# Optimization experiments

Measured on AMD Instinct MI355X. Metric: run time of the kernel, lower is better.

Reference implementation:

```python
import jax, jax.numpy as jnp
import numpy as np

FP8_MAX = 448.0  # float8_e4m3fn max (use_e4m3=True)
K, N = 512, 512


def setup_inputs() -> dict:
    key = jax.random.key(0)
    kx, kw = jax.random.split(key)
    x = jax.random.normal(kx, (8, 8192, K), dtype=jnp.float32)
    weight = jax.random.normal(kw, (K, N), dtype=jnp.float32) * 0.02
    return {"x": x, "weight": weight}


def reference(x, weight):
    B, S, _ = x.shape
    x2d = x.reshape(-1, K)  # [M, K]

    # dynamic per-tensor quantization of activations to fp8 e4m3
    x_amax = jnp.max(jnp.abs(x2d))
    x_scale = FP8_MAX / jnp.maximum(x_amax, 1e-12)
    x_fp8 = jnp.clip(x2d * x_scale, -FP8_MAX, FP8_MAX).astype(jnp.float8_e4m3fn)

    # dynamic per-tensor quantization of weight (transposed, as in source)
    w_amax = jnp.max(jnp.abs(weight))
    w_scale = FP8_MAX / jnp.maximum(w_amax, 1e-12)
    w_fp8 = jnp.clip(weight.T * w_scale, -FP8_MAX, FP8_MAX).astype(jnp.float8_e4m3fn)  # [N, K]

    # cast-up matmul then dequantize with combined inverse scale
    res = jnp.matmul(x_fp8.astype(jnp.float32), w_fp8.astype(jnp.float32).T)  # [M, N]
    out = res * ((1.0 / x_scale) * (1.0 / w_scale))
    return out.reshape(B, S, N).astype(x.dtype)
```

## Files before the change

### kernel.cpp

```cpp
#include <hip/hip_runtime.h>

typedef float f32x4 __attribute__((ext_vector_type(4)));
typedef long i64;

#define KDIM 512
#define NDIM 512
#define LDS_STRIDE 520
#define OUT_STRIDE 260

__device__ __forceinline__ float clamp448(float v) {
    return fminf(fmaxf(v, -448.0f), 448.0f);
}

__global__ __launch_bounds__(256) void amax_kernel(const float4* __restrict__ x,
                                                   const float4* __restrict__ w,
                                                   unsigned* __restrict__ scales) {
    const int tid = threadIdx.x;
    float m = 0.0f;
    if (blockIdx.x < 4096) {
        int base = blockIdx.x * 256 + tid;
        #pragma unroll
        for (int j = 0; j < 8; ++j) {
            float4 v = x[base + j * 1048576];
            m = fmaxf(m, fmaxf(fmaxf(fabsf(v.x), fabsf(v.y)), fmaxf(fabsf(v.z), fabsf(v.w))));
        }
    } else {
        int base = (blockIdx.x - 4096) * 256 + tid;
        #pragma unroll
        for (int j = 0; j < 8; ++j) {
            float4 v = w[base + j * 8192];
            m = fmaxf(m, fmaxf(fmaxf(fabsf(v.x), fabsf(v.y)), fmaxf(fabsf(v.z), fabsf(v.w))));
        }
    }
    #pragma unroll
    for (int off = 32; off > 0; off >>= 1)
        m = fmaxf(m, __shfl_down(m, off, 64));
    __shared__ float red[4];
    const int wave = tid >> 6, lane = tid & 63;
    if (lane == 0) red[wave] = m;
    __syncthreads();
    if (tid == 0) {
        m = fmaxf(fmaxf(red[0], red[1]), fmaxf(red[2], red[3]));
        atomicMax(&scales[blockIdx.x < 4096 ? 0 : 1], __float_as_uint(m));
    }
}

__global__ __launch_bounds__(256) void wquant_kernel(const float4* __restrict__ wv,
                                                     const unsigned* __restrict__ scales,
                                                     unsigned char* __restrict__ wq) {
    const float ws = 448.0f / fmaxf(__uint_as_float(scales[1]), 1e-12f);
    #pragma unroll
    for (int j = 0; j < 4; ++j) {
        const int idx = blockIdx.x * 1024 + j * 256 + threadIdx.x;
        const int k = idx >> 7;
        const int n4 = idx & 127;
        float4 v = wv[idx];
        float a[4] = {v.x, v.y, v.z, v.w};
        #pragma unroll
        for (int i = 0; i < 4; ++i) {
            float q = clamp448(a[i] * ws);
            int p = __builtin_amdgcn_cvt_pk_fp8_f32(q, q, 0, false);
            wq[(n4 * 4 + i) * KDIM + k] = (unsigned char)(p & 0xff);
        }
    }
}

__global__ __launch_bounds__(256, 4) void gemm_kernel(const float* __restrict__ x,
                                                      const unsigned char* __restrict__ wq,
                                                      const unsigned* __restrict__ scales,
                                                      float* __restrict__ out) {
    __shared__ unsigned char lds_a[64 * LDS_STRIDE];
    __shared__ float lds_o[16 * OUT_STRIDE];
    const int tid = threadIdx.x;
    const long m0 = (long)blockIdx.x * 64;

    const float ax = fmaxf(__uint_as_float(scales[0]), 1e-12f);
    const float aw = fmaxf(__uint_as_float(scales[1]), 1e-12f);
    const float xs = 448.0f / ax;
    const float ws = 448.0f / aw;
    const float inv = (1.0f / xs) * (1.0f / ws);

    const float4* xv = (const float4*)(x + m0 * KDIM);
    #pragma unroll 8
    for (int j = 0; j < 32; ++j) {
        int f4i = tid + 256 * j;
        float4 v = xv[f4i];
        int row = f4i >> 7;
        int colb = (f4i & 127) << 2;
        float a0 = clamp448(v.x * xs);
        float a1 = clamp448(v.y * xs);
        float a2 = clamp448(v.z * xs);
        float a3 = clamp448(v.w * xs);
        int p = __builtin_amdgcn_cvt_pk_fp8_f32(a0, a1, 0, false);
        p = __builtin_amdgcn_cvt_pk_fp8_f32(a2, a3, p, true);
        *(unsigned*)&lds_a[row * LDS_STRIDE + colb] = (unsigned)p;
    }
    __syncthreads();

    const int wave = tid >> 6, lane = tid & 63;
    const int ln = lane & 15, lg = lane >> 4;
    const int kofs = lg * 8;
    float* outp = out + m0 * NDIM;

    for (int chunk = 0; chunk < 2; ++chunk) {
        const int nbase = chunk * 256 + wave * 64;
        f32x4 acc[4][4];
        #pragma unroll
        for (int a = 0; a < 4; ++a)
            #pragma unroll
            for (int b = 0; b < 4; ++b)
                acc[a][b] = (f32x4){0.0f, 0.0f, 0.0f, 0.0f};

        for (int ks = 0; ks < 16; ++ks) {
            const int kb = ks * 32 + kofs;
            i64 af[4], bf[4];
            #pragma unroll
            for (int t = 0; t < 4; ++t)
                af[t] = *(const i64*)&lds_a[(t * 16 + ln) * LDS_STRIDE + kb];
            #pragma unroll
            for (int t = 0; t < 4; ++t)
                bf[t] = *(const i64*)&wq[(nbase + t * 16 + ln) * KDIM + kb];
            #pragma unroll
            for (int tm = 0; tm < 4; ++tm)
                #pragma unroll
                for (int tn = 0; tn < 4; ++tn)
                    acc[tm][tn] = __builtin_amdgcn_mfma_f32_16x16x32_fp8_fp8(
                        af[tm], bf[tn], acc[tm][tn], 0, 0, 0);
        }

        #pragma unroll 1
        for (int tm = 0; tm < 4; ++tm) {
            __syncthreads();
            #pragma unroll
            for (int tn = 0; tn < 4; ++tn) {
                const int c = wave * 64 + tn * 16 + ln;
                #pragma unroll
                for (int r = 0; r < 4; ++r)
                    lds_o[(lg * 4 + r) * OUT_STRIDE + c] = acc[tm][tn][r] * inv;
            }
            __syncthreads();
            #pragma unroll
            for (int j = 0; j < 4; ++j) {
                const int idx = j * 256 + tid;
                const int rr = idx >> 6;
                const int c4 = idx & 63;
                float4 v = *(const float4*)&lds_o[rr * OUT_STRIDE + c4 * 4];
                *(float4*)&outp[(long)(tm * 16 + rr) * NDIM + chunk * 256 + c4 * 4] = v;
            }
        }
    }
}

extern "C" void kernel_launch(void* const* d_in, const int* in_sizes, int n_in,
                              void* d_out, int out_size, void* d_ws, size_t ws_size,
                              hipStream_t stream) {
    const float* x = (const float*)d_in[0];
    const float* w = (const float*)d_in[1];
    float* out = (float*)d_out;
    unsigned* scales = (unsigned*)d_ws;
    unsigned char* wq = (unsigned char*)d_ws + 256;
    const int M = in_sizes[0] / KDIM;

    hipMemsetAsync(d_ws, 0, 8, stream);
    amax_kernel<<<4096 + 32, 256, 0, stream>>>((const float4*)x, (const float4*)w, scales);
    wquant_kernel<<<64, 256, 0, stream>>>((const float4*)w, scales, wq);
    gemm_kernel<<<M / 64, 256, 0, stream>>>(x, wq, scales, out);
}
```

Baseline: 357.9 us.

## Halve GEMM row tile to 32 and batch loads in amax and quant prologue

The GEMM block now covers 32 rows instead of 64, which doubles the grid and halves both LDS and accumulator use per block. This should raise occupancy and spread the work across more CUs, at the cost of loading the fp8 weight tile twice as often. The amax kernel now runs half as many blocks, each issuing 16 float4 loads up front before reducing. The GEMM prologue likewise issues all 16 float4 loads before converting, to expose more memory-level parallelism.

```diff
diff --git a/kernel.cpp b/kernel.cpp
--- a/kernel.cpp
+++ b/kernel.cpp
@@ -17,20 +17,24 @@
                                                    unsigned* __restrict__ scales) {
     const int tid = threadIdx.x;
     float m = 0.0f;
-    if (blockIdx.x < 4096) {
-        int base = blockIdx.x * 256 + tid;
+    if (blockIdx.x < 2048) {
+        const int base = blockIdx.x * 256 + tid;
+        float4 v[16];
         #pragma unroll
-        for (int j = 0; j < 8; ++j) {
-            float4 v = x[base + j * 1048576];
-            m = fmaxf(m, fmaxf(fmaxf(fabsf(v.x), fabsf(v.y)), fmaxf(fabsf(v.z), fabsf(v.w))));
-        }
+        for (int j = 0; j < 16; ++j) v[j] = x[base + j * 524288];
+        #pragma unroll
+        for (int j = 0; j < 16; ++j)
+            m = fmaxf(m, fmaxf(fmaxf(fabsf(v[j].x), fabsf(v[j].y)),
+                               fmaxf(fabsf(v[j].z), fabsf(v[j].w))));
     } else {
-        int base = (blockIdx.x - 4096) * 256 + tid;
+        const int base = (blockIdx.x - 2048) * 256 + tid;
+        float4 v[8];
         #pragma unroll
-        for (int j = 0; j < 8; ++j) {
-            float4 v = w[base + j * 8192];
-            m = fmaxf(m, fmaxf(fmaxf(fabsf(v.x), fabsf(v.y)), fmaxf(fabsf(v.z), fabsf(v.w))));
-        }
+        for (int j = 0; j < 8; ++j) v[j] = w[base + j * 8192];
+        #pragma unroll
+        for (int j = 0; j < 8; ++j)
+            m = fmaxf(m, fmaxf(fmaxf(fabsf(v[j].x), fabsf(v[j].y)),
+                               fmaxf(fabsf(v[j].z), fabsf(v[j].w))));
     }
     #pragma unroll
     for (int off = 32; off > 0; off >>= 1)
@@ -41,7 +45,7 @@
     __syncthreads();
     if (tid == 0) {
         m = fmaxf(fmaxf(red[0], red[1]), fmaxf(red[2], red[3]));
-        atomicMax(&scales[blockIdx.x < 4096 ? 0 : 1], __float_as_uint(m));
+        atomicMax(&scales[blockIdx.x < 2048 ? 0 : 1], __float_as_uint(m));
     }
 }
 
@@ -69,10 +73,10 @@
                                                       const unsigned char* __restrict__ wq,
                                                       const unsigned* __restrict__ scales,
                                                       float* __restrict__ out) {
-    __shared__ unsigned char lds_a[64 * LDS_STRIDE];
+    __shared__ unsigned char lds_a[32 * LDS_STRIDE];
     __shared__ float lds_o[16 * OUT_STRIDE];
     const int tid = threadIdx.x;
-    const long m0 = (long)blockIdx.x * 64;
+    const long m0 = (long)blockIdx.x * 32;
 
     const float ax = fmaxf(__uint_as_float(scales[0]), 1e-12f);
     const float aw = fmaxf(__uint_as_float(scales[1]), 1e-12f);
@@ -81,19 +85,23 @@
     const float inv = (1.0f / xs) * (1.0f / ws);
 
     const float4* xv = (const float4*)(x + m0 * KDIM);
-    #pragma unroll 8
-    for (int j = 0; j < 32; ++j) {
-        int f4i = tid + 256 * j;
-        float4 v = xv[f4i];
-        int row = f4i >> 7;
-        int colb = (f4i & 127) << 2;
-        float a0 = clamp448(v.x * xs);
-        float a1 = clamp448(v.y * xs);
-        float a2 = clamp448(v.z * xs);
-        float a3 = clamp448(v.w * xs);
-        int p = __builtin_amdgcn_cvt_pk_fp8_f32(a0, a1, 0, false);
-        p = __builtin_amdgcn_cvt_pk_fp8_f32(a2, a3, p, true);
-        *(unsigned*)&lds_a[row * LDS_STRIDE + colb] = (unsigned)p;
+    {
+        float4 v[16];
+        #pragma unroll
+        for (int j = 0; j < 16; ++j) v[j] = xv[tid + 256 * j];
+        #pragma unroll
+        for (int j = 0; j < 16; ++j) {
+            const int f4i = tid + 256 * j;
+            const int row = f4i >> 7;
+            const int colb = (f4i & 127) << 2;
+            float a0 = clamp448(v[j].x * xs);
+            float a1 = clamp448(v[j].y * xs);
+            float a2 = clamp448(v[j].z * xs);
+            float a3 = clamp448(v[j].w * xs);
+            int p = __builtin_amdgcn_cvt_pk_fp8_f32(a0, a1, 0, false);
+            p = __builtin_amdgcn_cvt_pk_fp8_f32(a2, a3, p, true);
+            *(unsigned*)&lds_a[row * LDS_STRIDE + colb] = (unsigned)p;
+        }
     }
     __syncthreads();
 
@@ -104,24 +112,24 @@
 
     for (int chunk = 0; chunk < 2; ++chunk) {
         const int nbase = chunk * 256 + wave * 64;
-        f32x4 acc[4][4];
+        f32x4 acc[2][4];
         #pragma unroll
-        for (int a = 0; a < 4; ++a)
+        for (int a = 0; a < 2; ++a)
             #pragma unroll
             for (int b = 0; b < 4; ++b)
                 acc[a][b] = (f32x4){0.0f, 0.0f, 0.0f, 0.0f};
 
         for (int ks = 0; ks < 16; ++ks) {
             const int kb = ks * 32 + kofs;
-            i64 af[4], bf[4];
+            i64 af[2], bf[4];
             #pragma unroll
-            for (int t = 0; t < 4; ++t)
+            for (int t = 0; t < 2; ++t)
                 af[t] = *(const i64*)&lds_a[(t * 16 + ln) * LDS_STRIDE + kb];
             #pragma unroll
             for (int t = 0; t < 4; ++t)
                 bf[t] = *(const i64*)&wq[(nbase + t * 16 + ln) * KDIM + kb];
             #pragma unroll
-            for (int tm = 0; tm < 4; ++tm)
+            for (int tm = 0; tm < 2; ++tm)
                 #pragma unroll
                 for (int tn = 0; tn < 4; ++tn)
                     acc[tm][tn] = __builtin_amdgcn_mfma_f32_16x16x32_fp8_fp8(
@@ -129,7 +137,7 @@
         }
 
         #pragma unroll 1
-        for (int tm = 0; tm < 4; ++tm) {
+        for (int tm = 0; tm < 2; ++tm) {
             __syncthreads();
             #pragma unroll
             for (int tn = 0; tn < 4; ++tn) {
@@ -162,7 +170,7 @@
     const int M = in_sizes[0] / KDIM;
 
     hipMemsetAsync(d_ws, 0, 8, stream);
-    amax_kernel<<<4096 + 32, 256, 0, stream>>>((const float4*)x, (const float4*)w, scales);
+    amax_kernel<<<2048 + 32, 256, 0, stream>>>((const float4*)x, (const float4*)w, scales);
     wquant_kernel<<<64, 256, 0, stream>>>((const float4*)w, scales, wq);
-    gemm_kernel<<<M / 64, 256, 0, stream>>>(x, wq, scales, out);
+    gemm_kernel<<<M / 32, 256, 0, stream>>>(x, wq, scales, out);
 }
```

Measured after the change: 387.0 us. +8.1%, slower.
